# Kernel optimization log

Hardware: AMD Instinct MI355X
Metric: run time of the kernel (lower is better)

The kernel has to match this reference:

```python
import jax, jax.numpy as jnp
import numpy as np

V, E, H, S = 32000, 1024, 1024, 2048


def setup_inputs() -> dict:
    key = jax.random.key(0)
    ks = jax.random.split(key, 16)
    std = 0.02
    return {
        "encoder_out": jax.random.normal(ks[0], (S, E), jnp.float32),
        "word_input": jax.random.randint(ks[1], (1,), 0, V, jnp.int32),
        "last_context": jax.random.normal(ks[2], (1, H), jnp.float32),
        "h0": jnp.zeros((1, 1, H), jnp.float32),
        "c0": jnp.zeros((1, 1, H), jnp.float32),
        # learned parameters
        "emb": jax.random.normal(ks[3], (V, E), jnp.float32) * std,
        "W_ih": jax.random.normal(ks[4], (4 * H, E + H), jnp.float32) * std,
        "W_hh": jax.random.normal(ks[5], (4 * H, H), jnp.float32) * std,
        "b_ih": jnp.zeros((4 * H,), jnp.float32),
        "b_hh": jnp.zeros((4 * H,), jnp.float32),
        "W_attn": jax.random.normal(ks[6], (H, E + H), jnp.float32) * std,
        "b_attn": jnp.zeros((H,), jnp.float32),
        "v": jax.random.uniform(ks[7], (H,), jnp.float32) * 0.1,
        "W_ah": jax.random.normal(ks[8], (H, E + H), jnp.float32) * std,
        "b_ah": jnp.zeros((H,), jnp.float32),
        "W_out": jax.random.normal(ks[9], (V, H), jnp.float32) * std,
        "b_out": jnp.zeros((V,), jnp.float32),
    }


def reference(encoder_out, word_input, last_context, h0, c0,
              emb, W_ih, W_hh, b_ih, b_hh,
              W_attn, b_attn, v, W_ah, b_ah, W_out, b_out):
    # single decoder step, batch=1 (dropout in eval mode == identity)
    embedded = emb[word_input[0]]                       # [E]
    x = jnp.concatenate([last_context[0], embedded])    # [H+E] (context first, as in torch.cat)
    # LSTM cell (PyTorch gate order i, f, g, o)
    gates = W_ih @ x + b_ih + W_hh @ h0[0, 0] + b_hh    # [4H]
    i, f, g, o = jnp.split(gates, 4)
    c = jax.nn.sigmoid(f) * c0[0, 0] + jax.nn.sigmoid(i) * jnp.tanh(g)
    ht = jax.nn.sigmoid(o) * jnp.tanh(c)                # [H]
    # additive attention, vectorized over encoder steps.
    # original concatenates (ht, encoder_out[i]); split attn weight accordingly.
    Wa_h, Wa_e = W_attn[:, :H], W_attn[:, H:]
    scores = jnp.tanh(encoder_out @ Wa_e.T + (Wa_h @ ht + b_attn)) @ v  # [S]
    w = jax.nn.softmax(scores)                          # [S]
    context = w @ encoder_out                           # [E]
    ht_tilda = jnp.tanh(W_ah @ jnp.concatenate([context, ht]) + b_ah)  # [H]
    output = jax.nn.log_softmax(W_out @ ht_tilda + b_out)              # [V]
    return (output[None, :], (ht[None, None, :], c[None, None, :]),
            ht_tilda[None, :], w[None, :])
```

## Files before the change

### kernel.cpp

```cpp
#include <hip/hip_runtime.h>
#include <math.h>

#define V_ 32000
#define E_ 1024
#define H_ 1024
#define S_ 2048

typedef __attribute__((ext_vector_type(8))) short bf16x8;
typedef __attribute__((ext_vector_type(8))) unsigned short u16x8;
typedef __attribute__((ext_vector_type(4))) float f32x4;

typedef __attribute__((address_space(1))) const unsigned int gu32;
typedef __attribute__((address_space(3))) unsigned int lu32;

__device__ __forceinline__ float sigmoidf_(float x) { return 1.0f / (1.0f + expf(-x)); }

__device__ __forceinline__ unsigned short f2bf(float f) {
    unsigned int u = __builtin_bit_cast(unsigned int, f);
    unsigned int r = (u + 0x7fffu + ((u >> 16) & 1u)) >> 16;
    return (unsigned short)r;
}

__device__ __forceinline__ u16x8 pack8(float4 a, float4 b) {
    u16x8 p;
    p[0] = f2bf(a.x); p[1] = f2bf(a.y); p[2] = f2bf(a.z); p[3] = f2bf(a.w);
    p[4] = f2bf(b.x); p[5] = f2bf(b.y); p[6] = f2bf(b.z); p[7] = f2bf(b.w);
    return p;
}

__device__ __forceinline__ void gload16(const void* g, void* l) {
    __builtin_amdgcn_global_load_lds((gu32*)g, (lu32*)l, 16, 0, 0);
}

__global__ __launch_bounds__(256) void k1_gates(
    const float* __restrict__ W_ih, const float* __restrict__ W_hh,
    const float* __restrict__ b_ih, const float* __restrict__ b_hh,
    const float* __restrict__ last_context, const float* __restrict__ emb,
    const int* __restrict__ word, const float* __restrict__ h0,
    const float* __restrict__ c0,
    float* __restrict__ out_ht, float* __restrict__ out_c,
    float* __restrict__ ws_ht)
{
    __shared__ float sbuf[4];
    int j = blockIdx.x;
    int tid = threadIdx.x, wave = tid >> 6, lane = tid & 63;
    const float* embrow = emb + (size_t)word[0] * E_;
    int row = j + wave * H_;
    const float* wi = W_ih + (size_t)row * (E_ + H_);
    const float* wh = W_hh + (size_t)row * H_;
    float acc = 0.f;
    #pragma unroll
    for (int it = 0; it < 8; ++it) {
        int idx = (lane + it * 64) * 4;
        float4 wv = *(const float4*)(wi + idx);
        float4 xv = (idx < H_) ? *(const float4*)(last_context + idx)
                               : *(const float4*)(embrow + (idx - H_));
        acc = fmaf(wv.x, xv.x, acc); acc = fmaf(wv.y, xv.y, acc);
        acc = fmaf(wv.z, xv.z, acc); acc = fmaf(wv.w, xv.w, acc);
    }
    #pragma unroll
    for (int it = 0; it < 4; ++it) {
        int idx = (lane + it * 64) * 4;
        float4 wv = *(const float4*)(wh + idx);
        float4 hv = *(const float4*)(h0 + idx);
        acc = fmaf(wv.x, hv.x, acc); acc = fmaf(wv.y, hv.y, acc);
        acc = fmaf(wv.z, hv.z, acc); acc = fmaf(wv.w, hv.w, acc);
    }
    #pragma unroll
    for (int m = 32; m; m >>= 1) acc += __shfl_down(acc, m, 64);
    if (lane == 0) sbuf[wave] = acc;
    __syncthreads();
    if (tid == 0) {
        float gi = sbuf[0] + b_ih[j]          + b_hh[j];
        float gf = sbuf[1] + b_ih[j + H_]     + b_hh[j + H_];
        float gg = sbuf[2] + b_ih[j + 2*H_]   + b_hh[j + 2*H_];
        float go = sbuf[3] + b_ih[j + 3*H_]   + b_hh[j + 3*H_];
        float c  = sigmoidf_(gf) * c0[j] + sigmoidf_(gi) * tanhf(gg);
        float ht = sigmoidf_(go) * tanhf(c);
        out_c[j]  = c;
        out_ht[j] = ht;
        ws_ht[j]  = ht;
    }
}

__global__ __launch_bounds__(64) void k2_q(
    const float* __restrict__ W_attn, const float* __restrict__ b_attn,
    const float* __restrict__ ht, float* __restrict__ q)
{
    int h = blockIdx.x;
    int lane = threadIdx.x;
    const float* row = W_attn + (size_t)h * (E_ + H_);
    float acc = 0.f;
    #pragma unroll
    for (int it = 0; it < 4; ++it) {
        int idx = (lane + it * 64) * 4;
        float4 wv = *(const float4*)(row + idx);
        float4 hv = *(const float4*)(ht + idx);
        acc = fmaf(wv.x, hv.x, acc); acc = fmaf(wv.y, hv.y, acc);
        acc = fmaf(wv.z, hv.z, acc); acc = fmaf(wv.w, hv.w, acc);
    }
    #pragma unroll
    for (int m = 32; m; m >>= 1) acc += __shfl_down(acc, m, 64);
    if (lane == 0) q[h] = acc + b_attn[h];
}

__global__ __launch_bounds__(256) void k3a_conv(
    const float* __restrict__ enc, const float* __restrict__ W_attn,
    unsigned short* __restrict__ encb, unsigned short* __restrict__ wab)
{
    int idx = blockIdx.x * 256 + threadIdx.x;
    const int ENC_CH = (S_ * E_) / 8;
    const float* src;
    unsigned short* dst;
    if (idx < ENC_CH) {
        src = enc + (size_t)idx * 8;
        dst = encb + (size_t)idx * 8;
    } else {
        int w = idx - ENC_CH;
        int h = w >> 7, off = (w & 127) * 8;
        src = W_attn + (size_t)h * (E_ + H_) + H_ + off;
        dst = wab + (size_t)h * E_ + off;
    }
    float4 a = *(const float4*)src;
    float4 b = *(const float4*)(src + 4);
    *(u16x8*)dst = pack8(a, b);
}

__global__ __launch_bounds__(256) void k3b_gemm(
    const unsigned short* __restrict__ encb, const unsigned short* __restrict__ wab,
    const float* __restrict__ q, const float* __restrict__ v,
    float* __restrict__ spart)
{
    __shared__ unsigned short As[2][128 * 64];
    __shared__ unsigned short Bs[2][64 * 64];
    int s0 = blockIdx.x * 128, h0 = blockIdx.y * 64;
    int tid = threadIdx.x;
    int wave = tid >> 6, lane = tid & 63;
    int wr = (wave >> 1) * 64, wc = (wave & 1) * 32;

    int srow = tid >> 3;
    int lch  = ((tid & 7) ^ (srow & 7)) * 8;
    const unsigned short* aSrc[4];
    #pragma unroll
    for (int jj = 0; jj < 4; ++jj)
        aSrc[jj] = encb + (size_t)(s0 + jj * 32 + srow) * E_ + lch;
    const unsigned short* bSrc[2];
    #pragma unroll
    for (int jj = 0; jj < 2; ++jj)
        bSrc[jj] = wab + (size_t)(h0 + jj * 32 + srow) * E_ + lch;

    int fc = lane & 15, g = lane >> 4;
    int aRow[4], bRow[2], pc[2];
    #pragma unroll
    for (int m = 0; m < 4; ++m) aRow[m] = (wr + m * 16 + fc) * 64;
    #pragma unroll
    for (int n = 0; n < 2; ++n) bRow[n] = (wc + n * 16 + fc) * 64;
    #pragma unroll
    for (int kk = 0; kk < 2; ++kk) pc[kk] = ((kk * 4 + g) ^ (fc & 7)) * 8;

    f32x4 acc[4][2];
    #pragma unroll
    for (int m = 0; m < 4; ++m)
        #pragma unroll
        for (int n = 0; n < 2; ++n)
            acc[m][n] = (f32x4){0.f, 0.f, 0.f, 0.f};

    #pragma unroll
    for (int jj = 0; jj < 4; ++jj) gload16(aSrc[jj], &As[0][jj * 2048 + tid * 8]);
    #pragma unroll
    for (int jj = 0; jj < 2; ++jj) gload16(bSrc[jj], &Bs[0][jj * 2048 + tid * 8]);
    __syncthreads();

    int cur = 0;
    for (int t = 0; t < 16; ++t) {
        if (t < 15) {
            int k0 = (t + 1) * 64;
            #pragma unroll
            for (int jj = 0; jj < 4; ++jj)
                gload16(aSrc[jj] + k0, &As[cur ^ 1][jj * 2048 + tid * 8]);
            #pragma unroll
            for (int jj = 0; jj < 2; ++jj)
                gload16(bSrc[jj] + k0, &Bs[cur ^ 1][jj * 2048 + tid * 8]);
        }
        #pragma unroll
        for (int kk = 0; kk < 2; ++kk) {
            bf16x8 af[4], bf2[2];
            #pragma unroll
            for (int m = 0; m < 4; ++m) af[m] = *(const bf16x8*)&As[cur][aRow[m] + pc[kk]];
            #pragma unroll
            for (int n = 0; n < 2; ++n) bf2[n] = *(const bf16x8*)&Bs[cur][bRow[n] + pc[kk]];
            #pragma unroll
            for (int m = 0; m < 4; ++m)
                #pragma unroll
                for (int n = 0; n < 2; ++n)
                    acc[m][n] = __builtin_amdgcn_mfma_f32_16x16x32_bf16(
                        af[m], bf2[n], acc[m][n], 0, 0, 0);
        }
        __syncthreads();
        cur ^= 1;
    }

    float qv[2], vv[2];
    #pragma unroll
    for (int n = 0; n < 2; ++n) {
        int col = h0 + wc + n * 16 + fc;
        qv[n] = q[col];
        vv[n] = v[col];
    }
    int part = blockIdx.y * 2 + (wave & 1);
    #pragma unroll
    for (int m = 0; m < 4; ++m) {
        #pragma unroll
        for (int j = 0; j < 4; ++j) {
            float p = 0.f;
            #pragma unroll
            for (int n = 0; n < 2; ++n)
                p += tanhf(acc[m][n][j] + qv[n]) * vv[n];
            #pragma unroll
            for (int mask = 8; mask; mask >>= 1) p += __shfl_xor(p, mask, 64);
            if (fc == 0)
                spart[(size_t)(s0 + wr + m * 16 + g * 4 + j) * 32 + part] = p;
        }
    }
}

__global__ __launch_bounds__(256) void k4_softmax(
    const float* __restrict__ spart, float* __restrict__ w_out,
    float* __restrict__ w_ws, float* __restrict__ ctx)
{
    __shared__ float sm[4];
    int tid = threadIdx.x;
    #pragma unroll
    for (int i = 0; i < 4; ++i) ctx[tid + i * 256] = 0.f;
    float x[8];
    float m = -1e30f;
    #pragma unroll
    for (int i = 0; i < 8; ++i) {
        int e = tid + i * 256;
        float acc = 0.f;
        #pragma unroll
        for (int c = 0; c < 8; ++c) {
            float4 pv = *(const float4*)&spart[(size_t)e * 32 + c * 4];
            acc += pv.x + pv.y + pv.z + pv.w;
        }
        x[i] = acc;
        m = fmaxf(m, acc);
    }
    #pragma unroll
    for (int s = 32; s; s >>= 1) m = fmaxf(m, __shfl_xor(m, s, 64));
    if ((tid & 63) == 0) sm[tid >> 6] = m;
    __syncthreads();
    m = fmaxf(fmaxf(sm[0], sm[1]), fmaxf(sm[2], sm[3]));
    float sum = 0.f;
    #pragma unroll
    for (int i = 0; i < 8; ++i) { x[i] = expf(x[i] - m); sum += x[i]; }
    #pragma unroll
    for (int s = 32; s; s >>= 1) sum += __shfl_xor(sum, s, 64);
    __syncthreads();
    if ((tid & 63) == 0) sm[tid >> 6] = sum;
    __syncthreads();
    sum = sm[0] + sm[1] + sm[2] + sm[3];
    float inv = 1.0f / sum;
    #pragma unroll
    for (int i = 0; i < 8; ++i) {
        float wv = x[i] * inv;
        w_out[tid + i * 256] = wv;
        w_ws[tid + i * 256]  = wv;
    }
}

__global__ __launch_bounds__(256) void k5_context(
    const float* __restrict__ enc, const float* __restrict__ w,
    float* __restrict__ context)
{
    int e = blockIdx.x * 256 + threadIdx.x;
    int s_begin = blockIdx.y * 64;
    float acc = 0.f;
    #pragma unroll 4
    for (int s = s_begin; s < s_begin + 64; ++s)
        acc = fmaf(w[s], enc[(size_t)s * E_ + e], acc);
    atomicAdd(&context[e], acc);
}

__global__ __launch_bounds__(64) void k6_htilda(
    const float* __restrict__ W_ah, const float* __restrict__ b_ah,
    const float* __restrict__ context, const float* __restrict__ ht,
    float* __restrict__ out_htt, float* __restrict__ ws_htt)
{
    int h = blockIdx.x;
    int lane = threadIdx.x;
    const float* row = W_ah + (size_t)h * (E_ + H_);
    float acc = 0.f;
    #pragma unroll
    for (int it = 0; it < 8; ++it) {
        int idx = (lane + it * 64) * 4;
        float4 wv = *(const float4*)(row + idx);
        float4 xv = (idx < E_) ? *(const float4*)(context + idx)
                               : *(const float4*)(ht + idx - E_);
        acc = fmaf(wv.x, xv.x, acc); acc = fmaf(wv.y, xv.y, acc);
        acc = fmaf(wv.z, xv.z, acc); acc = fmaf(wv.w, xv.w, acc);
    }
    #pragma unroll
    for (int m = 32; m; m >>= 1) acc += __shfl_down(acc, m, 64);
    if (lane == 0) {
        float val = tanhf(acc + b_ah[h]);
        out_htt[h] = val;
        ws_htt[h]  = val;
    }
}

__global__ __launch_bounds__(256) void k7_logits(
    const float* __restrict__ W_out, const float* __restrict__ b_out,
    const float* __restrict__ ht_tilda, float* __restrict__ logits)
{
    int row = blockIdx.x * 4 + (threadIdx.x >> 6);
    int lane = threadIdx.x & 63;
    const float* wr = W_out + (size_t)row * H_;
    float acc = 0.f;
    #pragma unroll
    for (int it = 0; it < 4; ++it) {
        int idx = (lane + it * 64) * 4;
        float4 wv = *(const float4*)(wr + idx);
        float4 hv = *(const float4*)(ht_tilda + idx);
        acc = fmaf(wv.x, hv.x, acc); acc = fmaf(wv.y, hv.y, acc);
        acc = fmaf(wv.z, hv.z, acc); acc = fmaf(wv.w, hv.w, acc);
    }
    #pragma unroll
    for (int m = 32; m; m >>= 1) acc += __shfl_down(acc, m, 64);
    if (lane == 0) logits[row] = acc + b_out[row];
}

__global__ __launch_bounds__(256) void k8_partial(
    const float* __restrict__ logits, float* __restrict__ part)
{
    __shared__ float smx[4], ssx[4];
    int b = blockIdx.x, tid = threadIdx.x;
    int base = b * 500;
    float m = -1e30f, s = 0.f;
    for (int i = tid; i < 500; i += 256) {
        float x = logits[base + i];
        float M = fmaxf(m, x);
        s = s * expf(m - M) + expf(x - M);
        m = M;
    }
    #pragma unroll
    for (int mask = 32; mask; mask >>= 1) {
        float om = __shfl_xor(m, mask, 64);
        float os = __shfl_xor(s, mask, 64);
        float M = fmaxf(m, om);
        s = s * expf(m - M) + os * expf(om - M);
        m = M;
    }
    if ((tid & 63) == 0) { smx[tid >> 6] = m; ssx[tid >> 6] = s; }
    __syncthreads();
    if (tid == 0) {
        float M = fmaxf(fmaxf(smx[0], smx[1]), fmaxf(smx[2], smx[3]));
        float S = ssx[0] * expf(smx[0] - M) + ssx[1] * expf(smx[1] - M)
                + ssx[2] * expf(smx[2] - M) + ssx[3] * expf(smx[3] - M);
        part[2 * b]     = M;
        part[2 * b + 1] = S;
    }
}

__global__ __launch_bounds__(256) void k9_finish(
    float* __restrict__ out, const float* __restrict__ part)
{
    __shared__ float slse;
    int tid = threadIdx.x;
    if (tid < 64) {
        float m = part[2 * tid], s = part[2 * tid + 1];
        #pragma unroll
        for (int mask = 32; mask; mask >>= 1) {
            float om = __shfl_xor(m, mask, 64);
            float os = __shfl_xor(s, mask, 64);
            float M = fmaxf(m, om);
            s = s * expf(m - M) + os * expf(om - M);
            m = M;
        }
        if (tid == 0) slse = m + logf(s);
    }
    __syncthreads();
    out[blockIdx.x * 256 + tid] -= slse;
}

extern "C" void kernel_launch(void* const* d_in, const int* in_sizes, int n_in,
                              void* d_out, int out_size, void* d_ws, size_t ws_size,
                              hipStream_t stream) {
    const float* enc          = (const float*)d_in[0];
    const int*   word         = (const int*)  d_in[1];
    const float* last_context = (const float*)d_in[2];
    const float* h0           = (const float*)d_in[3];
    const float* c0           = (const float*)d_in[4];
    const float* emb          = (const float*)d_in[5];
    const float* W_ih         = (const float*)d_in[6];
    const float* W_hh         = (const float*)d_in[7];
    const float* b_ih         = (const float*)d_in[8];
    const float* b_hh         = (const float*)d_in[9];
    const float* W_attn       = (const float*)d_in[10];
    const float* b_attn       = (const float*)d_in[11];
    const float* v            = (const float*)d_in[12];
    const float* W_ah         = (const float*)d_in[13];
    const float* b_ah         = (const float*)d_in[14];
    const float* W_out        = (const float*)d_in[15];
    const float* b_out        = (const float*)d_in[16];

    float* out        = (float*)d_out;
    float* out_logits = out;
    float* out_ht     = out + V_;
    float* out_c      = out + V_ + H_;
    float* out_htt    = out + V_ + 2 * H_;
    float* out_w      = out + V_ + 3 * H_;

    float* ws        = (float*)d_ws;
    float* ws_ht     = ws;
    float* ws_q      = ws + 1024;
    float* ws_w      = ws + 2048;
    float* ws_ctx    = ws + 4096;
    float* ws_htt    = ws + 5120;
    float* ws_part   = ws + 6144;
    float* ws_spart  = ws + 8192;
    unsigned short* encb = (unsigned short*)(ws + 73728);
    unsigned short* wab  = encb + (size_t)S_ * E_;

    k1_gates<<<1024, 256, 0, stream>>>(W_ih, W_hh, b_ih, b_hh, last_context, emb,
                                       word, h0, c0, out_ht, out_c, ws_ht);
    k2_q<<<1024, 64, 0, stream>>>(W_attn, b_attn, ws_ht, ws_q);
    k3a_conv<<<1536, 256, 0, stream>>>(enc, W_attn, encb, wab);
    k3b_gemm<<<dim3(S_ / 128, H_ / 64), 256, 0, stream>>>(encb, wab, ws_q, v, ws_spart);
    k4_softmax<<<1, 256, 0, stream>>>(ws_spart, out_w, ws_w, ws_ctx);
    k5_context<<<dim3(4, 32), 256, 0, stream>>>(enc, ws_w, ws_ctx);
    k6_htilda<<<1024, 64, 0, stream>>>(W_ah, b_ah, ws_ctx, ws_ht, out_htt, ws_htt);
    k7_logits<<<8000, 256, 0, stream>>>(W_out, b_out, ws_htt, out_logits);
    k8_partial<<<64, 256, 0, stream>>>(out_logits, ws_part);
    k9_finish<<<125, 256, 0, stream>>>(out_logits, ws_part);
}
```

Before: 91.90 us.

## Fuse all decoder stages into one cooperative persistent kernel with grid syncs

Replaces the ten separate kernel launches with a single cooperative kernel of 256 blocks that moves between stages using grid.sync. It overlaps the bf16 conversion with the LSTM gate GEMV, drops the max subtraction from both softmaxes (plain exp sums via atomics), and computes context from the bf16 encoder copy. The aim is to remove launch gaps and single-block serial stages such as the one-block softmax. In exchange it adds grid barrier costs, gives each stage less parallelism (the attention GEMM tiles shrink), and risks overflow in exp and lower precision in the context.

```diff
diff --git a/kernel.cpp b/kernel.cpp
--- a/kernel.cpp
+++ b/kernel.cpp
@@ -1,5 +1,8 @@
 #include <hip/hip_runtime.h>
+#include <hip/hip_cooperative_groups.h>
 #include <math.h>
+
+namespace cg = cooperative_groups;
 
 #define V_ 32000
 #define E_ 1024
@@ -20,417 +23,363 @@
     unsigned int r = (u + 0x7fffu + ((u >> 16) & 1u)) >> 16;
     return (unsigned short)r;
 }
-
+__device__ __forceinline__ float bf2f(unsigned short u) {
+    return __builtin_bit_cast(float, ((unsigned int)u) << 16);
+}
 __device__ __forceinline__ u16x8 pack8(float4 a, float4 b) {
     u16x8 p;
     p[0] = f2bf(a.x); p[1] = f2bf(a.y); p[2] = f2bf(a.z); p[3] = f2bf(a.w);
     p[4] = f2bf(b.x); p[5] = f2bf(b.y); p[6] = f2bf(b.z); p[7] = f2bf(b.w);
     return p;
 }
-
 __device__ __forceinline__ void gload16(const void* g, void* l) {
     __builtin_amdgcn_global_load_lds((gu32*)g, (lu32*)l, 16, 0, 0);
 }
 
-__global__ __launch_bounds__(256) void k1_gates(
-    const float* __restrict__ W_ih, const float* __restrict__ W_hh,
-    const float* __restrict__ b_ih, const float* __restrict__ b_hh,
-    const float* __restrict__ last_context, const float* __restrict__ emb,
-    const int* __restrict__ word, const float* __restrict__ h0,
-    const float* __restrict__ c0,
-    float* __restrict__ out_ht, float* __restrict__ out_c,
-    float* __restrict__ ws_ht)
+struct Params {
+    const float *enc, *last_context, *h0, *c0, *emb;
+    const float *W_ih, *W_hh, *b_ih, *b_hh;
+    const float *W_attn, *b_attn, *v, *W_ah, *b_ah, *W_out, *b_out;
+    const int* word;
+    float *out_logits, *out_ht, *out_c, *out_htt, *out_w;
+    float *ws_ht, *ws_q, *ws_expw, *ws_ctx, *ws_htt, *gS, *gSL, *spart;
+    unsigned short *encb, *wab;
+};
+
+__global__ __launch_bounds__(512) void mega(Params p)
 {
-    __shared__ float sbuf[4];
-    int j = blockIdx.x;
-    int tid = threadIdx.x, wave = tid >> 6, lane = tid & 63;
-    const float* embrow = emb + (size_t)word[0] * E_;
-    int row = j + wave * H_;
-    const float* wi = W_ih + (size_t)row * (E_ + H_);
-    const float* wh = W_hh + (size_t)row * H_;
-    float acc = 0.f;
-    #pragma unroll
-    for (int it = 0; it < 8; ++it) {
-        int idx = (lane + it * 64) * 4;
-        float4 wv = *(const float4*)(wi + idx);
-        float4 xv = (idx < H_) ? *(const float4*)(last_context + idx)
-                               : *(const float4*)(embrow + (idx - H_));
-        acc = fmaf(wv.x, xv.x, acc); acc = fmaf(wv.y, xv.y, acc);
-        acc = fmaf(wv.z, xv.z, acc); acc = fmaf(wv.w, xv.w, acc);
-    }
-    #pragma unroll
-    for (int it = 0; it < 4; ++it) {
-        int idx = (lane + it * 64) * 4;
-        float4 wv = *(const float4*)(wh + idx);
-        float4 hv = *(const float4*)(h0 + idx);
-        acc = fmaf(wv.x, hv.x, acc); acc = fmaf(wv.y, hv.y, acc);
-        acc = fmaf(wv.z, hv.z, acc); acc = fmaf(wv.w, hv.w, acc);
-    }
-    #pragma unroll
-    for (int m = 32; m; m >>= 1) acc += __shfl_down(acc, m, 64);
-    if (lane == 0) sbuf[wave] = acc;
-    __syncthreads();
-    if (tid == 0) {
-        float gi = sbuf[0] + b_ih[j]          + b_hh[j];
-        float gf = sbuf[1] + b_ih[j + H_]     + b_hh[j + H_];
-        float gg = sbuf[2] + b_ih[j + 2*H_]   + b_hh[j + 2*H_];
-        float go = sbuf[3] + b_ih[j + 3*H_]   + b_hh[j + 3*H_];
-        float c  = sigmoidf_(gf) * c0[j] + sigmoidf_(gi) * tanhf(gg);
-        float ht = sigmoidf_(go) * tanhf(c);
-        out_c[j]  = c;
-        out_ht[j] = ht;
-        ws_ht[j]  = ht;
-    }
-}
-
-__global__ __launch_bounds__(64) void k2_q(
-    const float* __restrict__ W_attn, const float* __restrict__ b_attn,
-    const float* __restrict__ ht, float* __restrict__ q)
-{
-    int h = blockIdx.x;
-    int lane = threadIdx.x;
-    const float* row = W_attn + (size_t)h * (E_ + H_);
-    float acc = 0.f;
-    #pragma unroll
-    for (int it = 0; it < 4; ++it) {
-        int idx = (lane + it * 64) * 4;
-        float4 wv = *(const float4*)(row + idx);
-        float4 hv = *(const float4*)(ht + idx);
-        acc = fmaf(wv.x, hv.x, acc); acc = fmaf(wv.y, hv.y, acc);
-        acc = fmaf(wv.z, hv.z, acc); acc = fmaf(wv.w, hv.w, acc);
-    }
-    #pragma unroll
-    for (int m = 32; m; m >>= 1) acc += __shfl_down(acc, m, 64);
-    if (lane == 0) q[h] = acc + b_attn[h];
-}
-
-__global__ __launch_bounds__(256) void k3a_conv(
-    const float* __restrict__ enc, const float* __restrict__ W_attn,
-    unsigned short* __restrict__ encb, unsigned short* __restrict__ wab)
-{
-    int idx = blockIdx.x * 256 + threadIdx.x;
-    const int ENC_CH = (S_ * E_) / 8;
-    const float* src;
-    unsigned short* dst;
-    if (idx < ENC_CH) {
-        src = enc + (size_t)idx * 8;
-        dst = encb + (size_t)idx * 8;
+    cg::grid_group grid = cg::this_grid();
+    __shared__ __attribute__((aligned(16))) unsigned char smem[49152];
+    const int b = blockIdx.x, tid = threadIdx.x;
+    const int wave = tid >> 6, lane = tid & 63;
+
+    if (wave < 4) {
+        int j = b * 4 + wave;
+        const float* embrow = p.emb + (size_t)p.word[0] * E_;
+        float g4[4];
+        #pragma unroll
+        for (int r = 0; r < 4; ++r) {
+            int row = j + r * H_;
+            const float* wi = p.W_ih + (size_t)row * (E_ + H_);
+            const float* wh = p.W_hh + (size_t)row * H_;
+            float acc = 0.f;
+            #pragma unroll
+            for (int it = 0; it < 8; ++it) {
+                int idx = (lane + it * 64) * 4;
+                float4 wv = *(const float4*)(wi + idx);
+                float4 xv = (idx < H_) ? *(const float4*)(p.last_context + idx)
+                                       : *(const float4*)(embrow + (idx - H_));
+                acc = fmaf(wv.x, xv.x, acc); acc = fmaf(wv.y, xv.y, acc);
+                acc = fmaf(wv.z, xv.z, acc); acc = fmaf(wv.w, xv.w, acc);
+            }
+            #pragma unroll
+            for (int it = 0; it < 4; ++it) {
+                int idx = (lane + it * 64) * 4;
+                float4 wv = *(const float4*)(wh + idx);
+                float4 hv = *(const float4*)(p.h0 + idx);
+                acc = fmaf(wv.x, hv.x, acc); acc = fmaf(wv.y, hv.y, acc);
+                acc = fmaf(wv.z, hv.z, acc); acc = fmaf(wv.w, hv.w, acc);
+            }
+            #pragma unroll
+            for (int m = 32; m; m >>= 1) acc += __shfl_down(acc, m, 64);
+            g4[r] = acc;
+        }
+        if (lane == 0) {
+            float gi = g4[0] + p.b_ih[j]          + p.b_hh[j];
+            float gf = g4[1] + p.b_ih[j + H_]     + p.b_hh[j + H_];
+            float gg = g4[2] + p.b_ih[j + 2*H_]   + p.b_hh[j + 2*H_];
+            float go = g4[3] + p.b_ih[j + 3*H_]   + p.b_hh[j + 3*H_];
+            float c  = sigmoidf_(gf) * p.c0[j] + sigmoidf_(gi) * tanhf(gg);
+            float ht = sigmoidf_(go) * tanhf(c);
+            p.out_c[j]  = c;
+            p.out_ht[j] = ht;
+            p.ws_ht[j]  = ht;
+        }
     } else {
-        int w = idx - ENC_CH;
-        int h = w >> 7, off = (w & 127) * 8;
-        src = W_attn + (size_t)h * (E_ + H_) + H_ + off;
-        dst = wab + (size_t)h * E_ + off;
-    }
-    float4 a = *(const float4*)src;
-    float4 b = *(const float4*)(src + 4);
-    *(u16x8*)dst = pack8(a, b);
-}
-
-__global__ __launch_bounds__(256) void k3b_gemm(
-    const unsigned short* __restrict__ encb, const unsigned short* __restrict__ wab,
-    const float* __restrict__ q, const float* __restrict__ v,
-    float* __restrict__ spart)
-{
-    __shared__ unsigned short As[2][128 * 64];
-    __shared__ unsigned short Bs[2][64 * 64];
-    int s0 = blockIdx.x * 128, h0 = blockIdx.y * 64;
-    int tid = threadIdx.x;
-    int wave = tid >> 6, lane = tid & 63;
-    int wr = (wave >> 1) * 64, wc = (wave & 1) * 32;
-
-    int srow = tid >> 3;
-    int lch  = ((tid & 7) ^ (srow & 7)) * 8;
-    const unsigned short* aSrc[4];
-    #pragma unroll
-    for (int jj = 0; jj < 4; ++jj)
-        aSrc[jj] = encb + (size_t)(s0 + jj * 32 + srow) * E_ + lch;
-    const unsigned short* bSrc[2];
-    #pragma unroll
-    for (int jj = 0; jj < 2; ++jj)
-        bSrc[jj] = wab + (size_t)(h0 + jj * 32 + srow) * E_ + lch;
-
-    int fc = lane & 15, g = lane >> 4;
-    int aRow[4], bRow[2], pc[2];
-    #pragma unroll
-    for (int m = 0; m < 4; ++m) aRow[m] = (wr + m * 16 + fc) * 64;
-    #pragma unroll
-    for (int n = 0; n < 2; ++n) bRow[n] = (wc + n * 16 + fc) * 64;
-    #pragma unroll
-    for (int kk = 0; kk < 2; ++kk) pc[kk] = ((kk * 4 + g) ^ (fc & 7)) * 8;
-
-    f32x4 acc[4][2];
-    #pragma unroll
-    for (int m = 0; m < 4; ++m)
-        #pragma unroll
-        for (int n = 0; n < 2; ++n)
-            acc[m][n] = (f32x4){0.f, 0.f, 0.f, 0.f};
-
-    #pragma unroll
-    for (int jj = 0; jj < 4; ++jj) gload16(aSrc[jj], &As[0][jj * 2048 + tid * 8]);
-    #pragma unroll
-    for (int jj = 0; jj < 2; ++jj) gload16(bSrc[jj], &Bs[0][jj * 2048 + tid * 8]);
-    __syncthreads();
-
-    int cur = 0;
-    for (int t = 0; t < 16; ++t) {
-        if (t < 15) {
-            int k0 = (t + 1) * 64;
-            #pragma unroll
-            for (int jj = 0; jj < 4; ++jj)
-                gload16(aSrc[jj] + k0, &As[cur ^ 1][jj * 2048 + tid * 8]);
-            #pragma unroll
-            for (int jj = 0; jj < 2; ++jj)
-                gload16(bSrc[jj] + k0, &Bs[cur ^ 1][jj * 2048 + tid * 8]);
-        }
-        #pragma unroll
-        for (int kk = 0; kk < 2; ++kk) {
-            bf16x8 af[4], bf2[2];
-            #pragma unroll
-            for (int m = 0; m < 4; ++m) af[m] = *(const bf16x8*)&As[cur][aRow[m] + pc[kk]];
-            #pragma unroll
-            for (int n = 0; n < 2; ++n) bf2[n] = *(const bf16x8*)&Bs[cur][bRow[n] + pc[kk]];
-            #pragma unroll
-            for (int m = 0; m < 4; ++m)
+        int cid = (b * 4 + (wave - 4)) * 64 + lane;
+        const int ENC_CH = (S_ * E_) / 8;
+        #pragma unroll
+        for (int i = 0; i < 6; ++i) {
+            int idx = cid + i * 65536;
+            const float* src;
+            unsigned short* dst;
+            if (idx < ENC_CH) {
+                src = p.enc + (size_t)idx * 8;
+                dst = p.encb + (size_t)idx * 8;
+            } else {
+                int w = idx - ENC_CH;
+                int h = w >> 7, off = (w & 127) * 8;
+                src = p.W_attn + (size_t)h * (E_ + H_) + H_ + off;
+                dst = p.wab + (size_t)h * E_ + off;
+            }
+            float4 a = *(const float4*)src;
+            float4 bq = *(const float4*)(src + 4);
+            *(u16x8*)dst = pack8(a, bq);
+        }
+    }
+    if (b == 0) {
+        p.ws_ctx[tid] = 0.f;
+        p.ws_ctx[tid + 512] = 0.f;
+        if (tid == 0) { *p.gS = 0.f; *p.gSL = 0.f; }
+    }
+    grid.sync();
+
+    if (wave < 4) {
+        int h = b * 4 + wave;
+        const float* row = p.W_attn + (size_t)h * (E_ + H_);
+        float acc = 0.f;
+        #pragma unroll
+        for (int it = 0; it < 4; ++it) {
+            int idx = (lane + it * 64) * 4;
+            float4 wv = *(const float4*)(row + idx);
+            float4 hv = *(const float4*)(p.ws_ht + idx);
+            acc = fmaf(wv.x, hv.x, acc); acc = fmaf(wv.y, hv.y, acc);
+            acc = fmaf(wv.z, hv.z, acc); acc = fmaf(wv.w, hv.w, acc);
+        }
+        #pragma unroll
+        for (int m = 32; m; m >>= 1) acc += __shfl_down(acc, m, 64);
+        if (lane == 0) p.ws_q[h] = acc + p.b_attn[h];
+    }
+    grid.sync();
+
+    {
+        unsigned short* As = (unsigned short*)smem;
+        unsigned short* Bs = (unsigned short*)(smem + 32768);
+        int bx = b & 15, by = b >> 4;
+        int s0 = bx * 128, h0 = by * 64;
+        int srow = tid >> 3;
+        int lch  = ((tid & 7) ^ (srow & 7)) * 8;
+        const unsigned short* aSrc0 = p.encb + (size_t)(s0 + srow) * E_ + lch;
+        const unsigned short* aSrc1 = p.encb + (size_t)(s0 + 64 + srow) * E_ + lch;
+        const unsigned short* bSrc  = p.wab  + (size_t)(h0 + srow) * E_ + lch;
+
+        int wr = (wave >> 1) * 32, wc = (wave & 1) * 32;
+        int fc = lane & 15, g = lane >> 4;
+        int aRow[2], bRow[2], pc[2];
+        #pragma unroll
+        for (int m = 0; m < 2; ++m) aRow[m] = (wr + m * 16 + fc) * 64;
+        #pragma unroll
+        for (int n = 0; n < 2; ++n) bRow[n] = (wc + n * 16 + fc) * 64;
+        #pragma unroll
+        for (int kk = 0; kk < 2; ++kk) pc[kk] = ((kk * 4 + g) ^ (fc & 7)) * 8;
+
+        f32x4 acc[2][2];
+        #pragma unroll
+        for (int m = 0; m < 2; ++m)
+            #pragma unroll
+            for (int n = 0; n < 2; ++n)
+                acc[m][n] = (f32x4){0.f, 0.f, 0.f, 0.f};
+
+        gload16(aSrc0, As + tid * 8);
+        gload16(aSrc1, As + (tid + 512) * 8);
+        gload16(bSrc,  Bs + tid * 8);
+        __syncthreads();
+
+        int cur = 0;
+        for (int t = 0; t < 16; ++t) {
+            if (t < 15) {
+                int k0 = (t + 1) * 64;
+                gload16(aSrc0 + k0, As + (cur ^ 1) * 8192 + tid * 8);
+                gload16(aSrc1 + k0, As + (cur ^ 1) * 8192 + (tid + 512) * 8);
+                gload16(bSrc  + k0, Bs + (cur ^ 1) * 4096 + tid * 8);
+            }
+            #pragma unroll
+            for (int kk = 0; kk < 2; ++kk) {
+                bf16x8 af[2], bf2[2];
+                #pragma unroll
+                for (int m = 0; m < 2; ++m)
+                    af[m] = *(const bf16x8*)(As + cur * 8192 + aRow[m] + pc[kk]);
                 #pragma unroll
                 for (int n = 0; n < 2; ++n)
-                    acc[m][n] = __builtin_amdgcn_mfma_f32_16x16x32_bf16(
-                        af[m], bf2[n], acc[m][n], 0, 0, 0);
+                    bf2[n] = *(const bf16x8*)(Bs + cur * 4096 + bRow[n] + pc[kk]);
+                #pragma unroll
+                for (int m = 0; m < 2; ++m)
+                    #pragma unroll
+                    for (int n = 0; n < 2; ++n)
+                        acc[m][n] = __builtin_amdgcn_mfma_f32_16x16x32_bf16(
+                            af[m], bf2[n], acc[m][n], 0, 0, 0);
+            }
+            __syncthreads();
+            cur ^= 1;
+        }
+
+        float qv[2], vv[2];
+        #pragma unroll
+        for (int n = 0; n < 2; ++n) {
+            int col = h0 + wc + n * 16 + fc;
+            qv[n] = p.ws_q[col];
+            vv[n] = p.v[col];
+        }
+        int part = by * 2 + (wave & 1);
+        #pragma unroll
+        for (int m = 0; m < 2; ++m) {
+            #pragma unroll
+            for (int j = 0; j < 4; ++j) {
+                float pp = 0.f;
+                #pragma unroll
+                for (int n = 0; n < 2; ++n)
+                    pp += tanhf(acc[m][n][j] + qv[n]) * vv[n];
+                #pragma unroll
+                for (int mask = 8; mask; mask >>= 1) pp += __shfl_xor(pp, mask, 64);
+                if (fc == 0)
+                    p.spart[(size_t)(s0 + wr + m * 16 + g * 4 + j) * 32 + part] = pp;
+            }
+        }
+    }
+    grid.sync();
+
+    {
+        float* sred = (float*)smem;
+        int s = b * 8 + wave;
+        float val = 0.f;
+        if (lane < 32) val = p.spart[(size_t)s * 32 + lane];
+        #pragma unroll
+        for (int mask = 16; mask; mask >>= 1) val += __shfl_xor(val, mask, 64);
+        if (lane == 0) {
+            float e = expf(val);
+            p.ws_expw[s] = e;
+            sred[wave] = e;
         }
         __syncthreads();
-        cur ^= 1;
-    }
-
-    float qv[2], vv[2];
-    #pragma unroll
-    for (int n = 0; n < 2; ++n) {
-        int col = h0 + wc + n * 16 + fc;
-        qv[n] = q[col];
-        vv[n] = v[col];
-    }
-    int part = blockIdx.y * 2 + (wave & 1);
-    #pragma unroll
-    for (int m = 0; m < 4; ++m) {
-        #pragma unroll
-        for (int j = 0; j < 4; ++j) {
-            float p = 0.f;
-            #pragma unroll
-            for (int n = 0; n < 2; ++n)
-                p += tanhf(acc[m][n][j] + qv[n]) * vv[n];
-            #pragma unroll
-            for (int mask = 8; mask; mask >>= 1) p += __shfl_xor(p, mask, 64);
-            if (fc == 0)
-                spart[(size_t)(s0 + wr + m * 16 + g * 4 + j) * 32 + part] = p;
-        }
-    }
-}
-
-__global__ __launch_bounds__(256) void k4_softmax(
-    const float* __restrict__ spart, float* __restrict__ w_out,
-    float* __restrict__ w_ws, float* __restrict__ ctx)
-{
-    __shared__ float sm[4];
-    int tid = threadIdx.x;
-    #pragma unroll
-    for (int i = 0; i < 4; ++i) ctx[tid + i * 256] = 0.f;
-    float x[8];
-    float m = -1e30f;
-    #pragma unroll
-    for (int i = 0; i < 8; ++i) {
-        int e = tid + i * 256;
+        if (tid == 0) {
+            float bs = 0.f;
+            #pragma unroll
+            for (int i = 0; i < 8; ++i) bs += sred[i];
+            atomicAdd(p.gS, bs);
+        }
+    }
+    grid.sync();
+
+    {
+        float invS = 1.0f / (*p.gS);
+        if (b == 0) {
+            #pragma unroll
+            for (int i = 0; i < 4; ++i) {
+                int s = tid + i * 512;
+                p.out_w[s] = p.ws_expw[s] * invS;
+            }
+        }
+        int ex = b & 3, sg = b >> 2;
+        int e = ex * 256 + (tid & 255), shalf = tid >> 8;
+        int sbase = sg * 32 + shalf * 16;
         float acc = 0.f;
         #pragma unroll
-        for (int c = 0; c < 8; ++c) {
-            float4 pv = *(const float4*)&spart[(size_t)e * 32 + c * 4];
-            acc += pv.x + pv.y + pv.z + pv.w;
-        }
-        x[i] = acc;
-        m = fmaxf(m, acc);
-    }
-    #pragma unroll
-    for (int s = 32; s; s >>= 1) m = fmaxf(m, __shfl_xor(m, s, 64));
-    if ((tid & 63) == 0) sm[tid >> 6] = m;
-    __syncthreads();
-    m = fmaxf(fmaxf(sm[0], sm[1]), fmaxf(sm[2], sm[3]));
-    float sum = 0.f;
-    #pragma unroll
-    for (int i = 0; i < 8; ++i) { x[i] = expf(x[i] - m); sum += x[i]; }
-    #pragma unroll
-    for (int s = 32; s; s >>= 1) sum += __shfl_xor(sum, s, 64);
-    __syncthreads();
-    if ((tid & 63) == 0) sm[tid >> 6] = sum;
-    __syncthreads();
-    sum = sm[0] + sm[1] + sm[2] + sm[3];
-    float inv = 1.0f / sum;
-    #pragma unroll
-    for (int i = 0; i < 8; ++i) {
-        float wv = x[i] * inv;
-        w_out[tid + i * 256] = wv;
-        w_ws[tid + i * 256]  = wv;
-    }
-}
-
-__global__ __launch_bounds__(256) void k5_context(
-    const float* __restrict__ enc, const float* __restrict__ w,
-    float* __restrict__ context)
-{
-    int e = blockIdx.x * 256 + threadIdx.x;
-    int s_begin = blockIdx.y * 64;
-    float acc = 0.f;
-    #pragma unroll 4
-    for (int s = s_begin; s < s_begin + 64; ++s)
-        acc = fmaf(w[s], enc[(size_t)s * E_ + e], acc);
-    atomicAdd(&context[e], acc);
-}
-
-__global__ __launch_bounds__(64) void k6_htilda(
-    const float* __restrict__ W_ah, const float* __restrict__ b_ah,
-    const float* __restrict__ context, const float* __restrict__ ht,
-    float* __restrict__ out_htt, float* __restrict__ ws_htt)
-{
-    int h = blockIdx.x;
-    int lane = threadIdx.x;
-    const float* row = W_ah + (size_t)h * (E_ + H_);
-    float acc = 0.f;
-    #pragma unroll
-    for (int it = 0; it < 8; ++it) {
-        int idx = (lane + it * 64) * 4;
-        float4 wv = *(const float4*)(row + idx);
-        float4 xv = (idx < E_) ? *(const float4*)(context + idx)
-                               : *(const float4*)(ht + idx - E_);
-        acc = fmaf(wv.x, xv.x, acc); acc = fmaf(wv.y, xv.y, acc);
-        acc = fmaf(wv.z, xv.z, acc); acc = fmaf(wv.w, xv.w, acc);
-    }
-    #pragma unroll
-    for (int m = 32; m; m >>= 1) acc += __shfl_down(acc, m, 64);
-    if (lane == 0) {
-        float val = tanhf(acc + b_ah[h]);
-        out_htt[h] = val;
-        ws_htt[h]  = val;
-    }
-}
-
-__global__ __launch_bounds__(256) void k7_logits(
-    const float* __restrict__ W_out, const float* __restrict__ b_out,
-    const float* __restrict__ ht_tilda, float* __restrict__ logits)
-{
-    int row = blockIdx.x * 4 + (threadIdx.x >> 6);
-    int lane = threadIdx.x & 63;
-    const float* wr = W_out + (size_t)row * H_;
-    float acc = 0.f;
-    #pragma unroll
-    for (int it = 0; it < 4; ++it) {
-        int idx = (lane + it * 64) * 4;
-        float4 wv = *(const float4*)(wr + idx);
-        float4 hv = *(const float4*)(ht_tilda + idx);
-        acc = fmaf(wv.x, hv.x, acc); acc = fmaf(wv.y, hv.y, acc);
-        acc = fmaf(wv.z, hv.z, acc); acc = fmaf(wv.w, hv.w, acc);
-    }
-    #pragma unroll
-    for (int m = 32; m; m >>= 1) acc += __shfl_down(acc, m, 64);
-    if (lane == 0) logits[row] = acc + b_out[row];
-}
-
-__global__ __launch_bounds__(256) void k8_partial(
-    const float* __restrict__ logits, float* __restrict__ part)
-{
-    __shared__ float smx[4], ssx[4];
-    int b = blockIdx.x, tid = threadIdx.x;
-    int base = b * 500;
-    float m = -1e30f, s = 0.f;
-    for (int i = tid; i < 500; i += 256) {
-        float x = logits[base + i];
-        float M = fmaxf(m, x);
-        s = s * expf(m - M) + expf(x - M);
-        m = M;
-    }
-    #pragma unroll
-    for (int mask = 32; mask; mask >>= 1) {
-        float om = __shfl_xor(m, mask, 64);
-        float os = __shfl_xor(s, mask, 64);
-        float M = fmaxf(m, om);
-        s = s * expf(m - M) + os * expf(om - M);
-        m = M;
-    }
-    if ((tid & 63) == 0) { smx[tid >> 6] = m; ssx[tid >> 6] = s; }
-    __syncthreads();
-    if (tid == 0) {
-        float M = fmaxf(fmaxf(smx[0], smx[1]), fmaxf(smx[2], smx[3]));
-        float S = ssx[0] * expf(smx[0] - M) + ssx[1] * expf(smx[1] - M)
-                + ssx[2] * expf(smx[2] - M) + ssx[3] * expf(smx[3] - M);
-        part[2 * b]     = M;
-        part[2 * b + 1] = S;
-    }
-}
-
-__global__ __launch_bounds__(256) void k9_finish(
-    float* __restrict__ out, const float* __restrict__ part)
-{
-    __shared__ float slse;
-    int tid = threadIdx.x;
-    if (tid < 64) {
-        float m = part[2 * tid], s = part[2 * tid + 1];
-        #pragma unroll
-        for (int mask = 32; mask; mask >>= 1) {
-            float om = __shfl_xor(m, mask, 64);
-            float os = __shfl_xor(s, mask, 64);
-            float M = fmaxf(m, om);
-            s = s * expf(m - M) + os * expf(om - M);
-            m = M;
-        }
-        if (tid == 0) slse = m + logf(s);
-    }
-    __syncthreads();
-    out[blockIdx.x * 256 + tid] -= slse;
+        for (int ss = 0; ss < 16; ++ss) {
+            int s = sbase + ss;
+            acc = fmaf(p.ws_expw[s] * invS, bf2f(p.encb[(size_t)s * E_ + e]), acc);
+        }
+        atomicAdd(&p.ws_ctx[e], acc);
+    }
+    grid.sync();
+
+    if (wave < 4) {
+        int h = b * 4 + wave;
+        const float* row = p.W_ah + (size_t)h * (E_ + H_);
+        float acc = 0.f;
+        #pragma unroll
+        for (int it = 0; it < 8; ++it) {
+            int idx = (lane + it * 64) * 4;
+            float4 wv = *(const float4*)(row + idx);
+            float4 xv = (idx < E_) ? *(const float4*)(p.ws_ctx + idx)
+                                   : *(const float4*)(p.ws_ht + (idx - E_));
+            acc = fmaf(wv.x, xv.x, acc); acc = fmaf(wv.y, xv.y, acc);
+            acc = fmaf(wv.z, xv.z, acc); acc = fmaf(wv.w, xv.w, acc);
+        }
+        #pragma unroll
+        for (int m = 32; m; m >>= 1) acc += __shfl_down(acc, m, 64);
+        if (lane == 0) {
+            float val = tanhf(acc + p.b_ah[h]);
+            p.out_htt[h] = val;
+            p.ws_htt[h]  = val;
+        }
+    }
+    grid.sync();
+
+    {
+        float* wes = (float*)smem;
+        int rbase = b * 125;
+        float esum = 0.f;
+        for (int r = 0; r < 16; ++r) {
+            int rl = wave * 16 + r;
+            if (rl < 125) {
+                int row = rbase + rl;
+                const float* wrp = p.W_out + (size_t)row * H_;
+                float acc = 0.f;
+                #pragma unroll
+                for (int it = 0; it < 4; ++it) {
+                    int idx = (lane + it * 64) * 4;
+                    float4 wv = *(const float4*)(wrp + idx);
+                    float4 hv = *(const float4*)(p.ws_htt + idx);
+                    acc = fmaf(wv.x, hv.x, acc); acc = fmaf(wv.y, hv.y, acc);
+                    acc = fmaf(wv.z, hv.z, acc); acc = fmaf(wv.w, hv.w, acc);
+                }
+                #pragma unroll
+                for (int m = 32; m; m >>= 1) acc += __shfl_down(acc, m, 64);
+                if (lane == 0) {
+                    float lg = acc + p.b_out[row];
+                    p.out_logits[row] = lg;
+                    esum += expf(lg);
+                }
+            }
+        }
+        if (lane == 0) wes[wave] = esum;
+        __syncthreads();
+        if (tid == 0) {
+            float bs = 0.f;
+            #pragma unroll
+            for (int i = 0; i < 8; ++i) bs += wes[i];
+            atomicAdd(p.gSL, bs);
+        }
+    }
+    grid.sync();
+
+    {
+        float lse = logf(*p.gSL);
+        if (tid < 125) p.out_logits[b * 125 + tid] -= lse;
+    }
 }
 
 extern "C" void kernel_launch(void* const* d_in, const int* in_sizes, int n_in,
                               void* d_out, int out_size, void* d_ws, size_t ws_size,
                               hipStream_t stream) {
-    const float* enc          = (const float*)d_in[0];
-    const int*   word         = (const int*)  d_in[1];
-    const float* last_context = (const float*)d_in[2];
-    const float* h0           = (const float*)d_in[3];
-    const float* c0           = (const float*)d_in[4];
-    const float* emb          = (const float*)d_in[5];
-    const float* W_ih         = (const float*)d_in[6];
-    const float* W_hh         = (const float*)d_in[7];
-    const float* b_ih         = (const float*)d_in[8];
-    const float* b_hh         = (const float*)d_in[9];
-    const float* W_attn       = (const float*)d_in[10];
-    const float* b_attn       = (const float*)d_in[11];
-    const float* v            = (const float*)d_in[12];
-    const float* W_ah         = (const float*)d_in[13];
-    const float* b_ah         = (const float*)d_in[14];
-    const float* W_out        = (const float*)d_in[15];
-    const float* b_out        = (const float*)d_in[16];
-
-    float* out        = (float*)d_out;
-    float* out_logits = out;
-    float* out_ht     = out + V_;
-    float* out_c      = out + V_ + H_;
-    float* out_htt    = out + V_ + 2 * H_;
-    float* out_w      = out + V_ + 3 * H_;
-
-    float* ws        = (float*)d_ws;
-    float* ws_ht     = ws;
-    float* ws_q      = ws + 1024;
-    float* ws_w      = ws + 2048;
-    float* ws_ctx    = ws + 4096;
-    float* ws_htt    = ws + 5120;
-    float* ws_part   = ws + 6144;
-    float* ws_spart  = ws + 8192;
-    unsigned short* encb = (unsigned short*)(ws + 73728);
-    unsigned short* wab  = encb + (size_t)S_ * E_;
-
-    k1_gates<<<1024, 256, 0, stream>>>(W_ih, W_hh, b_ih, b_hh, last_context, emb,
-                                       word, h0, c0, out_ht, out_c, ws_ht);
-    k2_q<<<1024, 64, 0, stream>>>(W_attn, b_attn, ws_ht, ws_q);
-    k3a_conv<<<1536, 256, 0, stream>>>(enc, W_attn, encb, wab);
-    k3b_gemm<<<dim3(S_ / 128, H_ / 64), 256, 0, stream>>>(encb, wab, ws_q, v, ws_spart);
-    k4_softmax<<<1, 256, 0, stream>>>(ws_spart, out_w, ws_w, ws_ctx);
-    k5_context<<<dim3(4, 32), 256, 0, stream>>>(enc, ws_w, ws_ctx);
-    k6_htilda<<<1024, 64, 0, stream>>>(W_ah, b_ah, ws_ctx, ws_ht, out_htt, ws_htt);
-    k7_logits<<<8000, 256, 0, stream>>>(W_out, b_out, ws_htt, out_logits);
-    k8_partial<<<64, 256, 0, stream>>>(out_logits, ws_part);
-    k9_finish<<<125, 256, 0, stream>>>(out_logits, ws_part);
-}
+    Params prm;
+    prm.enc          = (const float*)d_in[0];
+    prm.word         = (const int*)  d_in[1];
+    prm.last_context = (const float*)d_in[2];
+    prm.h0           = (const float*)d_in[3];
+    prm.c0           = (const float*)d_in[4];
+    prm.emb          = (const float*)d_in[5];
+    prm.W_ih         = (const float*)d_in[6];
+    prm.W_hh         = (const float*)d_in[7];
+    prm.b_ih         = (const float*)d_in[8];
+    prm.b_hh         = (const float*)d_in[9];
+    prm.W_attn       = (const float*)d_in[10];
+    prm.b_attn       = (const float*)d_in[11];
+    prm.v            = (const float*)d_in[12];
+    prm.W_ah         = (const float*)d_in[13];
+    prm.b_ah         = (const float*)d_in[14];
+    prm.W_out        = (const float*)d_in[15];
+    prm.b_out        = (const float*)d_in[16];
+
+    float* out = (float*)d_out;
+    prm.out_logits = out;
+    prm.out_ht     = out + V_;
+    prm.out_c      = out + V_ + H_;
+    prm.out_htt    = out + V_ + 2 * H_;
+    prm.out_w      = out + V_ + 3 * H_;
+
+    float* ws = (float*)d_ws;
+    prm.ws_ht   = ws;
+    prm.ws_q    = ws + 1024;
+    prm.ws_expw = ws + 2048;
+    prm.ws_ctx  = ws + 4096;
+    prm.ws_htt  = ws + 5120;
+    prm.gS      = ws + 6144;
+    prm.gSL     = ws + 6145;
+    prm.spart   = ws + 8192;
+    prm.encb    = (unsigned short*)(ws + 73728);
+    prm.wab     = prm.encb + (size_t)S_ * E_;
+
+    void* args[] = { &prm };
+    hipLaunchCooperativeKernel((void*)mega, dim3(256), dim3(512), args, 0, stream);
+}
```

New measurement: 247.9 us. +169.8%, slower.
